# Optimization experiments

Hardware: AMD Instinct MI355X
Metric: run time of the kernel (lower is better)

Reference implementation:

```python
import jax, jax.numpy as jnp
import numpy as np
import math

EMBED = 1024
HEADS = 16
HEAD_DIM = EMBED // HEADS


def setup_inputs() -> dict:
    key = jax.random.key(0)
    ks = jax.random.split(key, 6)
    scale = 1.0 / math.sqrt(EMBED)
    x = jax.random.normal(ks[0], (4, 2048, EMBED), dtype=jnp.float32)
    Wv = jax.random.normal(ks[1], (EMBED, EMBED), dtype=jnp.float32) * scale
    Wk = jax.random.normal(ks[2], (EMBED, EMBED), dtype=jnp.float32) * scale
    Wq = jax.random.normal(ks[3], (EMBED, EMBED), dtype=jnp.float32) * scale
    Wo = jax.random.normal(ks[4], (EMBED, EMBED), dtype=jnp.float32) * scale
    bo = jax.random.normal(ks[5], (EMBED,), dtype=jnp.float32) * 0.02
    return {"x": x, "Wq": Wq, "Wk": Wk, "Wv": Wv, "Wo": Wo, "bo": bo}


def reference(x, Wq, Wk, Wv, Wo, bo):
    N, S, E = x.shape
    H, D = HEADS, HEAD_DIM
    # Linear(E,E,bias=False): y = x @ W.T ; weights here stored as [out,in]
    q = (x @ Wq.T).reshape(N, S, H, D)
    k = (x @ Wk.T).reshape(N, S, H, D)
    v = (x @ Wv.T).reshape(N, S, H, D)
    energy = jnp.einsum('nqhd,nkhd->nhqk', q, k)  # [N,H,S,S]
    attn = jax.nn.softmax(energy / math.sqrt(D), axis=-1)
    out = jnp.einsum('nhql,nlhd->nqhd', attn, v).reshape(N, S, E)
    return out @ Wo.T + bo
```

## Files before the change

### kernel.cpp

```cpp
#include <hip/hip_runtime.h>
#include <stdint.h>

#define NB   4
#define SLEN 2048
#define EMB  1024
#define NH   16
#define HD   64
#define MTOT (NB * SLEN)

typedef __bf16 bf8_t  __attribute__((ext_vector_type(8)));
typedef __bf16 bf4_t  __attribute__((ext_vector_type(4)));
typedef float  f4_t   __attribute__((ext_vector_type(4)));

#if __has_builtin(__builtin_amdgcn_exp2f)
#define EXP2(x) __builtin_amdgcn_exp2f(x)
#else
#define EXP2(x) exp2f(x)
#endif

__device__ __forceinline__ void gld16(const void* g, void* l) {
    __builtin_amdgcn_global_load_lds(
        (__attribute__((address_space(1))) void*)(g),
        (__attribute__((address_space(3))) void*)(l),
        16, 0, 0);
}

__device__ __forceinline__ uint32_t pack_bf16_rtn(float a, float b) {
    uint32_t ua = __builtin_bit_cast(uint32_t, a) + 0x8000u;
    uint32_t ub = __builtin_bit_cast(uint32_t, b) + 0x8000u;
    return __builtin_amdgcn_perm(ub, ua, 0x07060302u);
}

__global__ __launch_bounds__(256) void cast_f2b(const float* __restrict__ s,
                                                __bf16* __restrict__ d, int n) {
    int i = (blockIdx.x * 256 + threadIdx.x) * 4;
    if (i >= n) return;
    float4 f = *(const float4*)(s + i);
    bf4_t o = { (__bf16)f.x, (__bf16)f.y, (__bf16)f.z, (__bf16)f.w };
    *(bf4_t*)(d + i) = o;
}

template <int MODE>
__global__ __launch_bounds__(256) void gemm_bt(const __bf16* __restrict__ A,
                                               const __bf16* __restrict__ B,
                                               void* __restrict__ Cv,
                                               const float* __restrict__ bias,
                                               int M, int N, int K) {
    __shared__ __bf16 As[128 * 64];
    __shared__ __bf16 Bs[128 * 64];

    const int tid  = threadIdx.x;
    const int lane = tid & 63;
    const int w    = tid >> 6;
    const int quad = lane >> 4;
    const int l16  = lane & 15;
    const int m0   = blockIdx.x * 128;
    const int n0   = blockIdx.y * 128;
    const int wm   = (w >> 1) * 64;
    const int wn   = (w & 1) * 64;

    f4_t acc[4][4];
#pragma unroll
    for (int i = 0; i < 4; ++i)
#pragma unroll
        for (int j = 0; j < 4; ++j) acc[i][j] = (f4_t){0.f, 0.f, 0.f, 0.f};

    for (int k0 = 0; k0 < K; k0 += 64) {
        __syncthreads();
#pragma unroll
        for (int t = 0; t < 4; ++t) {
            int c   = t * 256 + tid;
            int row = c >> 3;
            int kc  = (c & 7) ^ (row & 7);
            int cb  = c & ~63;
            gld16(A + (size_t)(m0 + row) * K + k0 + kc * 8, &As[cb * 8]);
            gld16(B + (size_t)(n0 + row) * K + k0 + kc * 8, &Bs[cb * 8]);
        }
        __syncthreads();
#pragma unroll
        for (int ks = 0; ks < 2; ++ks) {
            bf8_t af[4], bfr[4];
#pragma unroll
            for (int i = 0; i < 4; ++i) {
                int r = wm + i * 16 + l16;
                af[i] = *(const bf8_t*)&As[r * 64 + (((ks * 4 + quad) ^ (r & 7)) * 8)];
            }
#pragma unroll
            for (int j = 0; j < 4; ++j) {
                int r = wn + j * 16 + l16;
                bfr[j] = *(const bf8_t*)&Bs[r * 64 + (((ks * 4 + quad) ^ (r & 7)) * 8)];
            }
#pragma unroll
            for (int i = 0; i < 4; ++i)
#pragma unroll
                for (int j = 0; j < 4; ++j)
                    acc[i][j] = __builtin_amdgcn_mfma_f32_16x16x32_bf16(af[i], bfr[j],
                                                                        acc[i][j], 0, 0, 0);
        }
    }

#pragma unroll
    for (int i = 0; i < 4; ++i) {
#pragma unroll
        for (int j = 0; j < 4; ++j) {
            int m   = m0 + wm + i * 16 + quad * 4;
            int col = n0 + wn + j * 16 + l16;
            if (MODE == 0) {
                __bf16* Cb = (__bf16*)Cv;
#pragma unroll
                for (int r = 0; r < 4; ++r)
                    Cb[(size_t)(m + r) * N + col] = (__bf16)acc[i][j][r];
            } else if (MODE == 1) {
                __bf16* Cb = (__bf16*)Cv;
                size_t idx = ((size_t)(m >> 11) * 1024 + col) * 2048 + (m & 2047);
                bf4_t pk = { (__bf16)acc[i][j][0], (__bf16)acc[i][j][1],
                             (__bf16)acc[i][j][2], (__bf16)acc[i][j][3] };
                *(bf4_t*)&Cb[idx] = pk;
            } else {
                float* Cf = (float*)Cv;
#pragma unroll
                for (int r = 0; r < 4; ++r)
                    Cf[(size_t)(m + r) * N + col] = acc[i][j][r] + bias[col];
            }
        }
    }
}

__global__ __launch_bounds__(256, 4) void attn_fwd(const __bf16* __restrict__ Q,
                                                   const __bf16* __restrict__ K,
                                                   const __bf16* __restrict__ Vt,
                                                   __bf16* __restrict__ O) {
    __shared__ __bf16 Ks[64 * 64];
    __shared__ __bf16 Vs[64 * 64];
    __shared__ __bf16 Ps[4 * 32 * 72];

    const int tid  = threadIdx.x;
    const int lane = tid & 63;
    const int w    = tid >> 6;
    const int quad = lane >> 4;
    const int l16  = lane & 15;
    const int nh   = blockIdx.y;
    const int n    = nh >> 4;
    const int h    = nh & 15;
    const int q0   = blockIdx.x * 128 + w * 32;

    const float QSCALE = 0.125f * 1.44269504f;

    bf8_t bq[2][2];
#pragma unroll
    for (int jq = 0; jq < 2; ++jq)
#pragma unroll
        for (int ks = 0; ks < 2; ++ks) {
            bf8_t v = *(const bf8_t*)(Q + (size_t)(n * SLEN + q0 + jq * 16 + l16) * EMB +
                                      h * HD + ks * 32 + quad * 8);
#pragma unroll
            for (int t = 0; t < 8; ++t) v[t] = (__bf16)((float)v[t] * QSCALE);
            bq[jq][ks] = v;
        }

    float lsum[2] = {0.f, 0.f};
    f4_t o[2][4];
#pragma unroll
    for (int jq = 0; jq < 2; ++jq)
#pragma unroll
        for (int jd = 0; jd < 4; ++jd) o[jq][jd] = (f4_t){0.f, 0.f, 0.f, 0.f};

    const __bf16* kbase = K + (size_t)n * SLEN * EMB + h * HD;
    const __bf16* vbase = Vt + (size_t)nh * HD * SLEN;
    __bf16* pw = Ps + w * 32 * 72;
    const int sw = l16 & 7;

    for (int l0 = 0; l0 < SLEN; l0 += 64) {
        __syncthreads();
#pragma unroll
        for (int t = 0; t < 2; ++t) {
            int c   = t * 256 + tid;
            int row = c >> 3;
            int kc  = (c & 7) ^ (row & 7);
            int cb  = c & ~63;
            gld16(kbase + (size_t)(l0 + row) * EMB + kc * 8, &Ks[cb * 8]);
            gld16(vbase + (size_t)row * SLEN + l0 + kc * 8, &Vs[cb * 8]);
        }
        __syncthreads();

#pragma unroll
        for (int jk = 0; jk < 4; ++jk) {
            bf8_t ak[2];
#pragma unroll
            for (int ks = 0; ks < 2; ++ks)
                ak[ks] = *(const bf8_t*)&Ks[(jk * 16 + l16) * 64 +
                                            (((ks * 4 + quad) ^ sw) * 8)];
#pragma unroll
            for (int jq = 0; jq < 2; ++jq) {
                f4_t e = (f4_t){0.f, 0.f, 0.f, 0.f};
                e = __builtin_amdgcn_mfma_f32_16x16x32_bf16(ak[0], bq[jq][0], e, 0, 0, 0);
                e = __builtin_amdgcn_mfma_f32_16x16x32_bf16(ak[1], bq[jq][1], e, 0, 0, 0);
                float p0 = EXP2(e[0]), p1 = EXP2(e[1]);
                float p2 = EXP2(e[2]), p3 = EXP2(e[3]);
                lsum[jq] += (p0 + p1) + (p2 + p3);
                uint32_t d0 = pack_bf16_rtn(p0, p1);
                uint32_t d1 = pack_bf16_rtn(p2, p3);
                *(uint2*)&pw[(jq * 16 + l16) * 72 + jk * 16 + quad * 4] =
                    (uint2){d0, d1};
            }
        }

#pragma unroll
        for (int ks = 0; ks < 2; ++ks) {
            bf8_t bp[2];
#pragma unroll
            for (int jq = 0; jq < 2; ++jq)
                bp[jq] = *(const bf8_t*)&pw[(jq * 16 + l16) * 72 + ks * 32 + quad * 8];
#pragma unroll
            for (int jd = 0; jd < 4; ++jd) {
                bf8_t av = *(const bf8_t*)&Vs[(jd * 16 + l16) * 64 +
                                              (((ks * 4 + quad) ^ sw) * 8)];
#pragma unroll
                for (int jq = 0; jq < 2; ++jq)
                    o[jq][jd] = __builtin_amdgcn_mfma_f32_16x16x32_bf16(av, bp[jq],
                                                                        o[jq][jd], 0, 0, 0);
            }
        }
    }

#pragma unroll
    for (int jq = 0; jq < 2; ++jq) {
        float ls = lsum[jq];
        ls += __shfl_xor(ls, 16);
        ls += __shfl_xor(ls, 32);
        float inv = 1.0f / ls;
#pragma unroll
        for (int jd = 0; jd < 4; ++jd) {
            uint32_t d0 = pack_bf16_rtn(o[jq][jd][0] * inv, o[jq][jd][1] * inv);
            uint32_t d1 = pack_bf16_rtn(o[jq][jd][2] * inv, o[jq][jd][3] * inv);
            *(uint2*)&O[(size_t)(n * SLEN + q0 + jq * 16 + l16) * EMB + h * HD +
                        jd * 16 + quad * 4] = (uint2){d0, d1};
        }
    }
}

extern "C" void kernel_launch(void* const* d_in, const int* in_sizes, int n_in,
                              void* d_out, int out_size, void* d_ws, size_t ws_size,
                              hipStream_t stream) {
    const float* x  = (const float*)d_in[0];
    const float* Wq = (const float*)d_in[1];
    const float* Wk = (const float*)d_in[2];
    const float* Wv = (const float*)d_in[3];
    const float* Wo = (const float*)d_in[4];
    const float* bo = (const float*)d_in[5];

    char* wsb = (char*)d_ws;
    const size_t MB = (size_t)1 << 20;
    __bf16* xb  = (__bf16*)(wsb + 0 * MB);
    __bf16* ab  = xb;
    __bf16* wqb = (__bf16*)(wsb + 16 * MB);
    __bf16* wkb = (__bf16*)(wsb + 18 * MB);
    __bf16* wvb = (__bf16*)(wsb + 20 * MB);
    __bf16* wob = (__bf16*)(wsb + 22 * MB);
    __bf16* qb  = (__bf16*)(wsb + 24 * MB);
    __bf16* kb  = (__bf16*)(wsb + 40 * MB);
    __bf16* vtb = (__bf16*)(wsb + 56 * MB);

    const int NX = MTOT * EMB;
    const int NW = EMB * EMB;

    cast_f2b<<<dim3(NX / 1024), dim3(256), 0, stream>>>(x, xb, NX);
    cast_f2b<<<dim3(NW / 1024), dim3(256), 0, stream>>>(Wq, wqb, NW);
    cast_f2b<<<dim3(NW / 1024), dim3(256), 0, stream>>>(Wk, wkb, NW);
    cast_f2b<<<dim3(NW / 1024), dim3(256), 0, stream>>>(Wv, wvb, NW);
    cast_f2b<<<dim3(NW / 1024), dim3(256), 0, stream>>>(Wo, wob, NW);

    dim3 gg(MTOT / 128, EMB / 128);
    gemm_bt<0><<<gg, 256, 0, stream>>>(xb, wqb, qb, nullptr, MTOT, EMB, EMB);
    gemm_bt<0><<<gg, 256, 0, stream>>>(xb, wkb, kb, nullptr, MTOT, EMB, EMB);
    gemm_bt<1><<<gg, 256, 0, stream>>>(xb, wvb, vtb, nullptr, MTOT, EMB, EMB);

    attn_fwd<<<dim3(SLEN / 128, NB * NH), 256, 0, stream>>>(qb, kb, vtb, ab);

    gemm_bt<2><<<gg, 256, 0, stream>>>(ab, wob, d_out, bo, MTOT, EMB, EMB);
}
```

Measured before the change: 280.3 us.

## Fuse QKV projections into one GEMM, batch weight casts, MFMA row sums

Casts all four weight matrices in one launch into contiguous buffers, then runs the Q, K and V projections as a single GEMM with N=3072. The epilogue routes each column block to the Q, K or transposed-V destination. In attention, the softmax row sum is now computed by an MFMA with a ones vector over the bf16 P tile, replacing the scalar adds and cross-lane shuffles. P is also packed with truncation instead of round-to-nearest. These changes cut launch count and VALU work, at the cost of a small accuracy change from truncated P and from summing bf16-rounded probabilities.

```diff
diff --git a/kernel.cpp b/kernel.cpp
--- a/kernel.cpp
+++ b/kernel.cpp
@@ -29,6 +29,10 @@
     uint32_t ua = __builtin_bit_cast(uint32_t, a) + 0x8000u;
     uint32_t ub = __builtin_bit_cast(uint32_t, b) + 0x8000u;
     return __builtin_amdgcn_perm(ub, ua, 0x07060302u);
+}
+__device__ __forceinline__ uint32_t pack_bf16_rtz(float a, float b) {
+    return __builtin_amdgcn_perm(__builtin_bit_cast(uint32_t, b),
+                                 __builtin_bit_cast(uint32_t, a), 0x07060302u);
 }
 
 __global__ __launch_bounds__(256) void cast_f2b(const float* __restrict__ s,
@@ -38,6 +42,19 @@
     float4 f = *(const float4*)(s + i);
     bf4_t o = { (__bf16)f.x, (__bf16)f.y, (__bf16)f.z, (__bf16)f.w };
     *(bf4_t*)(d + i) = o;
+}
+
+__global__ __launch_bounds__(256) void cast_w4(const float* __restrict__ Wq,
+                                               const float* __restrict__ Wk,
+                                               const float* __restrict__ Wv,
+                                               const float* __restrict__ Wo,
+                                               __bf16* __restrict__ d) {
+    int y = blockIdx.y;
+    const float* s = (y == 0) ? Wq : (y == 1) ? Wk : (y == 2) ? Wv : Wo;
+    int i = (blockIdx.x * 256 + threadIdx.x) * 4;
+    float4 f = *(const float4*)(s + i);
+    bf4_t o = { (__bf16)f.x, (__bf16)f.y, (__bf16)f.z, (__bf16)f.w };
+    *(bf4_t*)(d + (size_t)y * (EMB * EMB) + i) = o;
 }
 
 template <int MODE>
@@ -105,22 +122,29 @@
         for (int j = 0; j < 4; ++j) {
             int m   = m0 + wm + i * 16 + quad * 4;
             int col = n0 + wn + j * 16 + l16;
-            if (MODE == 0) {
-                __bf16* Cb = (__bf16*)Cv;
-#pragma unroll
-                for (int r = 0; r < 4; ++r)
-                    Cb[(size_t)(m + r) * N + col] = (__bf16)acc[i][j][r];
-            } else if (MODE == 1) {
-                __bf16* Cb = (__bf16*)Cv;
-                size_t idx = ((size_t)(m >> 11) * 1024 + col) * 2048 + (m & 2047);
-                bf4_t pk = { (__bf16)acc[i][j][0], (__bf16)acc[i][j][1],
-                             (__bf16)acc[i][j][2], (__bf16)acc[i][j][3] };
-                *(bf4_t*)&Cb[idx] = pk;
-            } else {
+            if (MODE == 2) {
                 float* Cf = (float*)Cv;
 #pragma unroll
                 for (int r = 0; r < 4; ++r)
                     Cf[(size_t)(m + r) * N + col] = acc[i][j][r] + bias[col];
+            } else {
+                __bf16* qb = (__bf16*)Cv;
+                if (n0 < 1024) {
+#pragma unroll
+                    for (int r = 0; r < 4; ++r)
+                        qb[(size_t)(m + r) * 1024 + col] = (__bf16)acc[i][j][r];
+                } else if (n0 < 2048) {
+                    __bf16* kb = qb + (size_t)8 * 1024 * 1024;
+#pragma unroll
+                    for (int r = 0; r < 4; ++r)
+                        kb[(size_t)(m + r) * 1024 + (col - 1024)] = (__bf16)acc[i][j][r];
+                } else {
+                    __bf16* vtb = qb + (size_t)16 * 1024 * 1024;
+                    size_t idx = ((size_t)(m >> 11) * 1024 + (col - 2048)) * 2048 + (m & 2047);
+                    bf4_t pk = { (__bf16)acc[i][j][0], (__bf16)acc[i][j][1],
+                                 (__bf16)acc[i][j][2], (__bf16)acc[i][j][3] };
+                    *(bf4_t*)&vtb[idx] = pk;
+                }
             }
         }
     }
@@ -158,12 +182,18 @@
             bq[jq][ks] = v;
         }
 
-    float lsum[2] = {0.f, 0.f};
+    bf8_t aones;
+#pragma unroll
+    for (int t = 0; t < 8; ++t) aones[t] = (__bf16)1.0f;
+
+    f4_t ls[2];
     f4_t o[2][4];
 #pragma unroll
-    for (int jq = 0; jq < 2; ++jq)
+    for (int jq = 0; jq < 2; ++jq) {
+        ls[jq] = (f4_t){0.f, 0.f, 0.f, 0.f};
 #pragma unroll
         for (int jd = 0; jd < 4; ++jd) o[jq][jd] = (f4_t){0.f, 0.f, 0.f, 0.f};
+    }
 
     const __bf16* kbase = K + (size_t)n * SLEN * EMB + h * HD;
     const __bf16* vbase = Vt + (size_t)nh * HD * SLEN;
@@ -195,11 +225,8 @@
                 f4_t e = (f4_t){0.f, 0.f, 0.f, 0.f};
                 e = __builtin_amdgcn_mfma_f32_16x16x32_bf16(ak[0], bq[jq][0], e, 0, 0, 0);
                 e = __builtin_amdgcn_mfma_f32_16x16x32_bf16(ak[1], bq[jq][1], e, 0, 0, 0);
-                float p0 = EXP2(e[0]), p1 = EXP2(e[1]);
-                float p2 = EXP2(e[2]), p3 = EXP2(e[3]);
-                lsum[jq] += (p0 + p1) + (p2 + p3);
-                uint32_t d0 = pack_bf16_rtn(p0, p1);
-                uint32_t d1 = pack_bf16_rtn(p2, p3);
+                uint32_t d0 = pack_bf16_rtz(EXP2(e[0]), EXP2(e[1]));
+                uint32_t d1 = pack_bf16_rtz(EXP2(e[2]), EXP2(e[3]));
                 *(uint2*)&pw[(jq * 16 + l16) * 72 + jk * 16 + quad * 4] =
                     (uint2){d0, d1};
             }
@@ -211,6 +238,10 @@
 #pragma unroll
             for (int jq = 0; jq < 2; ++jq)
                 bp[jq] = *(const bf8_t*)&pw[(jq * 16 + l16) * 72 + ks * 32 + quad * 8];
+#pragma unroll
+            for (int jq = 0; jq < 2; ++jq)
+                ls[jq] = __builtin_amdgcn_mfma_f32_16x16x32_bf16(aones, bp[jq],
+                                                                 ls[jq], 0, 0, 0);
 #pragma unroll
             for (int jd = 0; jd < 4; ++jd) {
                 bf8_t av = *(const bf8_t*)&Vs[(jd * 16 + l16) * 64 +
@@ -225,10 +256,7 @@
 
 #pragma unroll
     for (int jq = 0; jq < 2; ++jq) {
-        float ls = lsum[jq];
-        ls += __shfl_xor(ls, 16);
-        ls += __shfl_xor(ls, 32);
-        float inv = 1.0f / ls;
+        float inv = 1.0f / ls[jq][0];
 #pragma unroll
         for (int jd = 0; jd < 4; ++jd) {
             uint32_t d0 = pack_bf16_rtn(o[jq][jd][0] * inv, o[jq][jd][1] * inv);
@@ -254,28 +282,22 @@
     __bf16* xb  = (__bf16*)(wsb + 0 * MB);
     __bf16* ab  = xb;
     __bf16* wqb = (__bf16*)(wsb + 16 * MB);
-    __bf16* wkb = (__bf16*)(wsb + 18 * MB);
-    __bf16* wvb = (__bf16*)(wsb + 20 * MB);
     __bf16* wob = (__bf16*)(wsb + 22 * MB);
     __bf16* qb  = (__bf16*)(wsb + 24 * MB);
-    __bf16* kb  = (__bf16*)(wsb + 40 * MB);
     __bf16* vtb = (__bf16*)(wsb + 56 * MB);
 
     const int NX = MTOT * EMB;
     const int NW = EMB * EMB;
 
     cast_f2b<<<dim3(NX / 1024), dim3(256), 0, stream>>>(x, xb, NX);
-    cast_f2b<<<dim3(NW / 1024), dim3(256), 0, stream>>>(Wq, wqb, NW);
-    cast_f2b<<<dim3(NW / 1024), dim3(256), 0, stream>>>(Wk, wkb, NW);
-    cast_f2b<<<dim3(NW / 1024), dim3(256), 0, stream>>>(Wv, wvb, NW);
-    cast_f2b<<<dim3(NW / 1024), dim3(256), 0, stream>>>(Wo, wob, NW);
-
-    dim3 gg(MTOT / 128, EMB / 128);
-    gemm_bt<0><<<gg, 256, 0, stream>>>(xb, wqb, qb, nullptr, MTOT, EMB, EMB);
-    gemm_bt<0><<<gg, 256, 0, stream>>>(xb, wkb, kb, nullptr, MTOT, EMB, EMB);
-    gemm_bt<1><<<gg, 256, 0, stream>>>(xb, wvb, vtb, nullptr, MTOT, EMB, EMB);
-
-    attn_fwd<<<dim3(SLEN / 128, NB * NH), 256, 0, stream>>>(qb, kb, vtb, ab);
-
-    gemm_bt<2><<<gg, 256, 0, stream>>>(ab, wob, d_out, bo, MTOT, EMB, EMB);
-}
+    cast_w4<<<dim3(NW / 1024, 4), dim3(256), 0, stream>>>(Wq, Wk, Wv, Wo, wqb);
+
+    gemm_bt<3><<<dim3(MTOT / 128, 3072 / 128), 256, 0, stream>>>(
+        xb, wqb, qb, nullptr, MTOT, 3072, EMB);
+
+    attn_fwd<<<dim3(SLEN / 128, NB * NH), 256, 0, stream>>>(qb, qb + (size_t)8 * MB,
+                                                            vtb, ab);
+
+    gemm_bt<2><<<dim3(MTOT / 128, EMB / 128), 256, 0, stream>>>(
+        ab, wob, d_out, bo, MTOT, EMB, EMB);
+}
```

New measurement: 270.2 us. -3.6%, faster.
